# Kernel optimization log

Hardware: AMD Instinct MI355X
Metric: run time of the kernel (lower is better)

The kernel has to match this reference:

```python
import jax, jax.numpy as jnp
import numpy as np

B, S, E, H, F = 4, 1024, 1024, 16, 4096
D = E // H
DEPTH = 3
EPS_LN = 1e-5
EPS_ENT = 1e-6


def setup_inputs() -> dict:
    key = jax.random.key(0)
    ks = jax.random.split(key, 32)
    def w(k, shp, s=0.02):
        return (jax.random.normal(k, shp) * s).astype(jnp.float32)
    z = lambda *shp: jnp.zeros(shp, jnp.float32)
    inp = {
        'x': jax.random.normal(ks[0], (B, S, E), jnp.float32),
        # self-referential attention
        'sr_w': w(ks[1], (E, E)), 'sr_b': z(E),
        'q_w': w(ks[2], (E, E)), 'q_b': z(E),
        'k_w': w(ks[3], (E, E)), 'k_b': z(E),
        'v_w': w(ks[4], (E, E)), 'v_b': z(E),
        'o_w': w(ks[5], (E, E)), 'o_b': z(E),
        'ref_gate': jnp.float32(0.5),
        # quantum-classical interface
        'c_w': w(ks[6], (E, E)), 'c_b': z(E),
        'qp_w': w(ks[7], (E, E)), 'qp_b': z(E),
        'ig_w': w(ks[8], (2 * E, E)), 'ig_b': z(E),
        'temperature': jnp.float32(1.0),
        # entropy regulator
        'kp_w': w(ks[9], (E, E)), 'kp_b': z(E),
        'ee_w': w(ks[10], (E, 1)), 'ee_b': z(1),
        'eta': jnp.float32(0.1),
        # ffn
        'f1_w': w(ks[11], (E, F)), 'f1_b': z(F),
        'f2_w': w(ks[12], (F, E)), 'f2_b': z(E),
        # layernorms
        'ln1_g': jnp.ones(E, jnp.float32), 'ln1_b': z(E),
        'ln2_g': jnp.ones(E, jnp.float32), 'ln2_b': z(E),
        'ln3_g': jnp.ones(E, jnp.float32), 'ln3_b': z(E),
        # observer
        'obs_w': w(ks[13], (E, E)), 'obs_b': z(E),
        'obs_gate': jnp.float32(0.2),
    }
    return inp


def _lin(x, W, b):
    return x @ W + b


def _ln(x, g, b):
    m = jnp.mean(x, -1, keepdims=True)
    v = jnp.var(x, -1, keepdims=True)
    return (x - m) * jax.lax.rsqrt(v + EPS_LN) * g + b


def _layer(x, p):
    ks = jax.lax.stop_gradient(x)  # knowledge_state = x.detach()
    scale = 1.0 / (D ** 0.5)
    for _ in range(DEPTH):  # fixed small recursion depth
        # --- self-referential attention on norm1(x) ---
        xn = _ln(x, p['ln1_g'], p['ln1_b'])
        xr = xn + p['ref_gate'] * _lin(xn, p['sr_w'], p['sr_b'])
        b, s, _ = xn.shape
        q = _lin(xr, p['q_w'], p['q_b']).reshape(b, s, H, D)
        k = _lin(xr, p['k_w'], p['k_b']).reshape(b, s, H, D)
        v = _lin(xn, p['v_w'], p['v_b']).reshape(b, s, H, D)
        scores = jnp.einsum('bqhd,bkhd->bhqk', q, k) * scale  # [B,H,S,S]
        aw = jax.nn.softmax(scores, axis=-1)
        ao = jnp.einsum('bhqk,bkhd->bqhd', aw, v).reshape(b, s, E)
        quantum = _lin(ao, p['o_w'], p['o_b'])
        # --- FFN on norm2(x) (dropout = identity, eval mode) ---
        xn2 = _ln(x, p['ln2_g'], p['ln2_b'])
        h = jax.nn.gelu(_lin(xn2, p['f1_w'], p['f1_b']), approximate=False)
        classical = _lin(h, p['f2_w'], p['f2_b'])
        # --- quantum-classical interface ---
        c_proj = _lin(classical, p['c_w'], p['c_b'])
        q_proj = _lin(quantum, p['qp_w'], p['qp_b'])
        gate = jax.nn.sigmoid(_lin(jnp.concatenate([c_proj, q_proj], -1), p['ig_w'], p['ig_b']))
        sim = jnp.einsum('bqe,bke->bqk', c_proj, q_proj) / (E ** 0.5)  # [B,S,S]
        attw = jax.nn.softmax(sim / p['temperature'], axis=-1)
        transfer = jnp.einsum('bqk,bke->bqe', attw, quantum)
        iface = classical + gate * transfer
        # --- entropy regulator ---
        logp = jax.nn.log_softmax(iface, axis=-1)
        entropy = -jnp.sum(jnp.exp(logp) * logp, -1, keepdims=True)
        neg_entropy = _lin(ks, p['kp_w'], p['kp_b'])
        bal = jax.nn.sigmoid(_lin(iface, p['ee_w'], p['ee_b']))
        regulated = iface + p['eta'] * bal * (neg_entropy / (entropy + EPS_ENT))
        # --- residual + observer feedback + knowledge update ---
        x = x + regulated
        x = x + p['obs_gate'] * _lin(x, p['obs_w'], p['obs_b'])
        ks = ks + 0.1 * (x - ks)
    x = _ln(x, p['ln3_g'], p['ln3_b'])
    return x, ks


def reference(x, sr_w, sr_b, q_w, q_b, k_w, k_b, v_w, v_b, o_w, o_b, ref_gate,
              c_w, c_b, qp_w, qp_b, ig_w, ig_b, temperature,
              kp_w, kp_b, ee_w, ee_b, eta,
              f1_w, f1_b, f2_w, f2_b,
              ln1_g, ln1_b, ln2_g, ln2_b, ln3_g, ln3_b,
              obs_w, obs_b, obs_gate):
    p = dict(sr_w=sr_w, sr_b=sr_b, q_w=q_w, q_b=q_b, k_w=k_w, k_b=k_b,
             v_w=v_w, v_b=v_b, o_w=o_w, o_b=o_b, ref_gate=ref_gate,
             c_w=c_w, c_b=c_b, qp_w=qp_w, qp_b=qp_b, ig_w=ig_w, ig_b=ig_b,
             temperature=temperature, kp_w=kp_w, kp_b=kp_b, ee_w=ee_w, ee_b=ee_b,
             eta=eta, f1_w=f1_w, f1_b=f1_b, f2_w=f2_w, f2_b=f2_b,
             ln1_g=ln1_g, ln1_b=ln1_b, ln2_g=ln2_g, ln2_b=ln2_b,
             ln3_g=ln3_g, ln3_b=ln3_b, obs_w=obs_w, obs_b=obs_b, obs_gate=obs_gate)
    return _layer(x, p)
```

## Files before the change

### kernel.cpp

```cpp
#include <hip/hip_runtime.h>
#include <hip/hip_bf16.h>
#include <cmath>


typedef unsigned short u16;
typedef short v8s __attribute__((ext_vector_type(8)));
typedef float v4f __attribute__((ext_vector_type(4)));
typedef unsigned short u16x4 __attribute__((ext_vector_type(4)));
typedef unsigned int u32x4 __attribute__((ext_vector_type(4)));

#define DEV __device__ __forceinline__

DEV float b2f(u16 u) { return __uint_as_float(((unsigned int)u) << 16); }
DEV u16 f2b(float f) {
    unsigned int x = __float_as_uint(f);
    return (u16)((x + 0x7fffu + ((x >> 16) & 1u)) >> 16);
}
DEV bool badf(float f) { return ((__float_as_uint(f) >> 23) & 0xFF) == 0xFF; }

DEV void async16(const void* g, void* l) {
    __builtin_amdgcn_global_load_lds((const __attribute__((address_space(1))) void*)g,
                                     (__attribute__((address_space(3))) void*)l, 16, 0, 0);
}

struct InArr { const void* p[37]; int n[37]; };
struct BJobs { int si[20]; int off[20]; int n[20]; };
struct GJ2 { const u16* jA; const u16* jB; const u16* jbias; u16* jout; };

#define CLS_CAP 16384

__global__ void reset_k(int* diag, int* cnt) {
    if (threadIdx.x == 0) *diag = 0x7FFFFFFF;
    if (threadIdx.x < 80) cnt[threadIdx.x] = 0;
}

__global__ void classify_k(InArr A, int* cnt) {
    int i = blockIdx.y;
    int n = A.n[i];
    if (n <= 1) return;
    long pairs = (long)n >> 1;
    int wild = 0, pz = 0;
    if (pairs > (long)(2 * CLS_CAP)) {
        const unsigned int* q32 = (const unsigned int*)A.p[i];
        long p0 = ((long)blockIdx.x * (pairs >> 3)) & ~3L;
        long tbase = p0 + (long)threadIdx.x * 8;
#pragma unroll
        for (int c = 0; c < 2; c++) {
            u32x4 v = *(const u32x4*)(q32 + tbase + c * 4);
#pragma unroll
            for (int j = 0; j < 4; j++) {
                unsigned int p = v[j];
                u16 w0 = (u16)(p & 0xFFFFu), w1 = (u16)(p >> 16);
                wild += ((w0 & 0x7FFF) >= 0x5000) + ((w1 & 0x7FFF) >= 0x5000);
                pz += (w0 == 0 && w1 >= 0x3000 && w1 <= 0x4100) ? 1 : 0;
            }
        }
    } else {
        const u16* q = (const u16*)A.p[i];
        long stride = (long)gridDim.x * blockDim.x;
        for (long j = (long)blockIdx.x * blockDim.x + threadIdx.x; j < pairs; j += stride) {
            u16 w0 = q[2 * j], w1 = q[2 * j + 1];
            wild += ((w0 & 0x7FFF) >= 0x5000) + ((w1 & 0x7FFF) >= 0x5000);
            pz += (w0 == 0 && w1 >= 0x3000 && w1 <= 0x4100) ? 1 : 0;
        }
    }
#pragma unroll
    for (int off = 1; off < 64; off <<= 1) {
        wild += __shfl_xor(wild, off);
        pz += __shfl_xor(pz, off);
    }
    if ((threadIdx.x & 63) == 0) {
        atomicAdd(&cnt[2 * i], wild);
        atomicAdd(&cnt[2 * i + 1], pz);
    }
}

__global__ void finalize_k(InArr A, const int* cnt, int* flags) {
    int i = threadIdx.x;
    if (i < 37) {
        int n = A.n[i];
        int f = 0;
        if (n > 1) {
            long pairs = (long)n >> 1;
            long wthr, pthr;
            if (pairs > (long)(2 * CLS_CAP)) { wthr = (2L * CLS_CAP) >> 6; pthr = (long)CLS_CAP >> 2; }
            else { wthr = (long)n >> 6; pthr = (long)n >> 3; }
            f = (cnt[2 * i] > wthr) || (cnt[2 * i + 1] > pthr);
        }
        flags[i] = f;
    }
}

DEV float dec_scalar(const u16* p) {
    float bf = b2f(p[0]);
    if (bf > 0.0009765625f && bf < 8.0f) return bf;
    unsigned int w = (((unsigned int)p[1]) << 16) | (unsigned int)p[0];
    return __uint_as_float(w);
}

__global__ void decode_scalars_k(const u16* rg, const u16* tp, const u16* et,
                                 const u16* og, float* out)
{
    if (threadIdx.x == 0 && blockIdx.x == 0) {
        out[0] = dec_scalar(rg);
        out[1] = dec_scalar(tp);
        out[2] = dec_scalar(et);
        out[3] = dec_scalar(og);
    }
}

__global__ void cvt1d_k(InArr A, BJobs J, const int* flags, u16* BIA) {
    int j = blockIdx.y;
    int n = J.n[j];
    int si = J.si[j];
    const void* src = A.p[si];
    u16* dst = BIA + (long)J.off[j] * 1024;
    int f = flags[si];
    int stride = gridDim.x * blockDim.x;
    for (int i = blockIdx.x * blockDim.x + threadIdx.x; i < n; i += stride) {
        dst[i] = f ? f2b(((const float*)src)[i]) : ((const u16*)src)[i];
    }
}

__global__ void chk_scal_k(const float* scal, int* diag) {
    if (threadIdx.x == 0) {
        for (int i = 0; i < 4; i++) {
            float v = scal[i];
            if (!(v > 0.f && v < 8.f)) atomicMin(diag, 3);
        }
    }
}

__global__ void fin32_k(float* out, long n4, const int* diag) {
    long stride = (long)gridDim.x * blockDim.x;
    long i0 = (long)blockIdx.x * blockDim.x + threadIdx.x;
    v4f* o4 = (v4f*)out;
    for (long i = i0; i < n4; i += stride) {
        v4f v = o4[i];
        bool b = false;
#pragma unroll
        for (int j = 0; j < 4; j++) b |= badf(v[j]);
        if (b) {
#pragma unroll
            for (int j = 0; j < 4; j++) if (badf(v[j])) v[j] = 0.f;
            o4[i] = v;
        }
    }
    if (i0 == 0) {
        int d = *diag;
        if (d != 0x7FFFFFFF) out[0] = 200.f + 4.f * (float)(d < 70 ? d : 70);
    }
}

__global__ void small_k(float* out, int code) {
    if (threadIdx.x == 0 && blockIdx.x == 0) out[0] = 900.f + 4.f * code;
}

__global__ __launch_bounds__(256) void f2c_k(const float* __restrict__ a, const float* __restrict__ b,
                                             const u16* __restrict__ bias, u16* __restrict__ out,
                                             int stage, int* __restrict__ diag)
{
    long i0 = ((long)blockIdx.x * 256 + threadIdx.x) * 4;
    v4f va = *(const v4f*)(a + i0);
    v4f vb = *(const v4f*)(b + i0);
    int colb = (int)(i0 & 1023);
    bool bad = false;
    u16x4 o;
#pragma unroll
    for (int j = 0; j < 4; j++) {
        float r = va[j] + vb[j] + b2f(bias[colb + j]);
        bad |= badf(r);
        o[j] = f2b(r);
    }
    *(u16x4*)(out + i0) = o;
    if (__ballot(bad) && (threadIdx.x & 63) == 0) atomicMin(diag, stage);
}

__global__ __launch_bounds__(256) void igc_k(const float* __restrict__ a, const float* __restrict__ b,
                                             const u16* __restrict__ bias, u16* __restrict__ out,
                                             int stage, int* __restrict__ diag)
{
    long i0 = ((long)blockIdx.x * 256 + threadIdx.x) * 4;
    v4f va = *(const v4f*)(a + i0);
    v4f vb = *(const v4f*)(b + i0);
    int colb = (int)(i0 & 1023);
    bool bad = false;
    u16x4 o;
#pragma unroll
    for (int j = 0; j < 4; j++) {
        float r = 1.f / (1.f + expf(-(va[j] + vb[j] + b2f(bias[colb + j]))));
        bad |= badf(r);
        o[j] = f2b(r);
    }
    *(u16x4*)(out + i0) = o;
    if (__ballot(bad) && (threadIdx.x & 63) == 0) atomicMin(diag, stage);
}

__global__ __launch_bounds__(256) void flashc_k(
    const float* __restrict__ Of, const float* __restrict__ Mf, const float* __restrict__ Lf,
    u16* __restrict__ ao, int stage, int* __restrict__ diag)
{
    long i0 = ((long)blockIdx.x * 256 + threadIdx.x) * 4;
    int row4 = (int)(i0 >> 10);
    int col = (int)(i0 & 1023);
    int b = row4 >> 10, srow = row4 & 1023, h = col >> 6;
    int mli = (((b << 4) + h) << 10) + srow;
    float m0 = Mf[mli], m1 = Mf[65536 + mli];
    float l0 = Lf[mli], l1 = Lf[65536 + mli];
    float m = fmaxf(m0, m1);
    float e0 = __expf(m0 - m), e1 = __expf(m1 - m);
    float inv = 1.f / (l0 * e0 + l1 * e1);
    v4f a = *(const v4f*)(Of + i0);
    v4f bb = *(const v4f*)(Of + 4194304 + i0);
    bool bad = false;
    u16x4 o;
#pragma unroll
    for (int j = 0; j < 4; j++) {
        float val = (a[j] * e0 + bb[j] * e1) * inv;
        bad |= badf(val);
        o[j] = f2b(val);
    }
    *(u16x4*)(ao + i0) = o;
    if (__ballot(bad) && (threadIdx.x & 63) == 0) atomicMin(diag, stage);
}

template <int EPI>
__global__ __launch_bounds__(512) void gemm_bt(
    const u16* __restrict__ A, int lda, long sA,
    const u16* __restrict__ A2, int ksplit,
    const u16* __restrict__ Bt, int ldb, long sB,
    const u16* __restrict__ bias,
    u16* __restrict__ obf, float* __restrict__ of32, int ldc, long sC,
    int K,
    const float* __restrict__ scp,
    const u16* __restrict__ aux,
    float* __restrict__ xaux, float* __restrict__ ksf, u16* __restrict__ ksb,
    float* __restrict__ kso,
    GJ2 J2,
    int stage, int* __restrict__ diag)
{
    __shared__ __align__(16) u16 As[128 * 64];
    __shared__ __align__(16) u16 Bs[128 * 64];
    const int tid = threadIdx.x;
    const int w = tid >> 6, l = tid & 63;
    const int lr = l & 15, lq = l >> 4;

    const int gx = gridDim.x, gy = gridDim.y;
    const int nwg = gx * gy * (int)gridDim.z;
    int flat = blockIdx.x + gx * (blockIdx.y + gy * blockIdx.z);
    int qq = nwg >> 3, rr = nwg & 7;
    int xcd = flat & 7, loc = flat >> 3;
    int nf = (xcd < rr ? xcd * (qq + 1) : rr * (qq + 1) + (xcd - rr) * qq) + loc;
    const int bx = nf % gx;
    int tmp = nf / gx;
    const int by = tmp % gy;
    int z = tmp / gy;

    const u16* Aj = A; const u16* Bj = Bt; const u16* biasj = bias; u16* obfj = obf;
    float* of32j = of32;
    if (J2.jA) {
        int jzs = (int)gridDim.z >> 1;
        if (z >= jzs) {
            Aj = J2.jA; Bj = J2.jB; biasj = J2.jbias;
            if (EPI == 8) of32j = (float*)J2.jout; else obfj = J2.jout;
            z -= jzs;
        }
    }

    const int m0 = by * 128, n0 = bx * 128;
    const u16* Az = Aj + (long)z * sA;
    const u16* Bz = Bj + (long)z * sB;
    const int wm = (w >> 2) * 64, wn = (w & 3) * 32;

    v4f zero4 = {0.f, 0.f, 0.f, 0.f};
    v4f acc[4][2];
#pragma unroll
    for (int i = 0; i < 4; i++)
#pragma unroll
        for (int j = 0; j < 2; j++) acc[i][j] = zero4;

    const int swz = lr & 7;
    const int c0s = (lq ^ swz) << 3;
    const int c1s = ((lq + 4) ^ swz) << 3;
    for (int k0 = 0; k0 < K; k0 += 64) {
        __syncthreads();
        const u16* Ab = (k0 < ksplit) ? (Az + k0) : (A2 + (k0 - ksplit));
#pragma unroll
        for (int p = 0; p < 2; p++) {
            int c = p * 512 + tid;
            int row = c >> 3;
            int sc = ((c & 7) ^ (row & 7)) * 8;
            async16(Ab + (long)(m0 + row) * lda + sc, (char*)As + p * 8192 + w * 1024);
            async16(Bz + (long)(n0 + row) * ldb + k0 + sc, (char*)Bs + p * 8192 + w * 1024);
        }
        __syncthreads();
        v8s av0[4], av1[4], bv0[2], bv1[2];
#pragma unroll
        for (int mi = 0; mi < 4; mi++) {
            const u16* Ar = As + ((wm + mi * 16 + lr) << 6);
            av0[mi] = *(const v8s*)(Ar + c0s);
            av1[mi] = *(const v8s*)(Ar + c1s);
        }
#pragma unroll
        for (int ni = 0; ni < 2; ni++) {
            const u16* Br = Bs + ((wn + ni * 16 + lr) << 6);
            bv0[ni] = *(const v8s*)(Br + c0s);
            bv1[ni] = *(const v8s*)(Br + c1s);
        }
#pragma unroll
        for (int mi = 0; mi < 4; mi++)
#pragma unroll
            for (int ni = 0; ni < 2; ni++)
                acc[mi][ni] = __builtin_amdgcn_mfma_f32_16x16x32_bf16(av0[mi], bv0[ni], acc[mi][ni], 0, 0, 0);
#pragma unroll
        for (int mi = 0; mi < 4; mi++)
#pragma unroll
            for (int ni = 0; ni < 2; ni++)
                acc[mi][ni] = __builtin_amdgcn_mfma_f32_16x16x32_bf16(av1[mi], bv1[ni], acc[mi][ni], 0, 0, 0);
    }

    float gsv = 0.f;
    if (EPI == 5 || EPI == 6) gsv = scp[0];
    bool bad = false;
#pragma unroll
    for (int mi = 0; mi < 4; mi++) {
        int row = m0 + wm + mi * 16 + lq * 4;
#pragma unroll
        for (int ni = 0; ni < 2; ni++) {
            int col = n0 + wn + ni * 16 + lr;
            float bb = biasj ? b2f(biasj[col]) : 0.f;
#pragma unroll
            for (int r = 0; r < 4; r++) {
                float v = acc[mi][ni][r] + bb;
                if (EPI == 6 || EPI == 7) {
                    long rbase = (long)(row + r) * 1024;
                    float res;
                    if (col < 1024) {
                        if (EPI == 6) res = b2f(aux[rbase + col]) + gsv * v;
                        else res = v * 0.125f;
                        bad |= badf(res);
                        obfj[rbase + col] = f2b(res);
                    } else {
                        res = v;
                        bad |= badf(res);
                        J2.jout[rbase + col - 1024] = f2b(res);
                    }
                } else {
                    long idx = (long)z * sC + (long)(row + r) * ldc + col;
                    float res = v;
                    if (EPI == 2) res = 0.5f * v * (1.f + erff(v * 0.70710678118654752f));
                    else if (EPI == 5) {
                        float xv = xaux[idx];
                        float nx = xv + gsv * v;
                        xaux[idx] = nx;
                        float kv = ksf[idx];
                        float kn = kv + 0.1f * (nx - kv);
                        ksf[idx] = kn;
                        ksb[idx] = f2b(kn);
                        if (kso) kso[idx] = kn;
                        bad |= badf(kn);
                        res = nx;
                    }
                    bad |= badf(res);
                    if (obfj) obfj[idx] = f2b(res);
                    if (of32j) of32j[idx] = res;
                }
            }
        }
    }
    if (__ballot(bad) && l == 0) atomicMin(diag, stage);
}

__global__ __launch_bounds__(256) void flash_k(
    const u16* __restrict__ q, const u16* __restrict__ k, const u16* __restrict__ v,
    float* __restrict__ Of, float* __restrict__ Mf, float* __restrict__ Lf)
{
    __shared__ __align__(16) u16 Ks[2 * 64 * 64];
    __shared__ __align__(16) u16 Vt[64 * 64];
    __shared__ __align__(16) u16 Pw[4 * 16 * 64];
    const int tid = threadIdx.x, w = tid >> 6, l = tid & 63;
    const int lr = l & 15, lq = l >> 4;
    const int flat = blockIdx.x + (blockIdx.y << 4) + (blockIdx.z << 10);
    const int xcd = flat & 7, loc = flat >> 3;
    const int bh = xcd * 8 + (loc >> 5);
    const int rest = loc & 31;
    const int zk = rest >> 4;
    const int q0 = (rest & 15) * 64;
    const int b = bh >> 4, h = bh & 15;
    const long rowbase = (long)b * 1024;
    const int h64 = h * 64;
    const long zoff = (long)zk << 19;

    const u16* Qp = q + (rowbase + q0 + w * 16 + lr) * 1024 + h64;
    v8s aq0 = *(const v8s*)(Qp + lq * 8);
    v8s aq1 = *(const v8s*)(Qp + 32 + lq * 8);

    v4f zero4 = {0.f, 0.f, 0.f, 0.f};
    v4f oacc[4];
    float m_r[4], l_r[4];
#pragma unroll
    for (int i = 0; i < 4; i++) { oacc[i] = zero4; m_r[i] = -INFINITY; l_r[i] = 0.f; }

    const int ss = lr & 7;
    const int colk = (lq ^ ss) << 3;
    u16* Pp = Pw + w * (16 * 64);

    const int c0 = tid, c1 = 256 + tid;
    const int row0 = c0 >> 3, cc0 = (c0 & 7) * 8;
    const int row1 = c1 >> 3, cc1 = (c1 & 7) * 8;
    const int sl0 = ((c0 & 7) ^ (row0 & 7)) * 8;
    const int sl1 = ((c1 & 7) ^ (row1 & 7)) * 8;
    int vt0[8], vt1[8];
#pragma unroll
    for (int j = 0; j < 8; j++) {
        int d0 = cc0 + j, g0 = (d0 & 7) ^ ((d0 >> 3) & 7);
        vt0[j] = ((d0 << 6) + row0) ^ (g0 << 3);
        int d1 = cc1 + j, g1 = (d1 & 7) ^ ((d1 >> 3) & 7);
        vt1[j] = ((d1 << 6) + row1) ^ (g1 << 3);
    }
    const u16* kc0 = k + (rowbase + row0) * 1024 + h64 + sl0 + zoff;
    const u16* kc1 = k + (rowbase + row1) * 1024 + h64 + sl1 + zoff;
    const u16* vc0 = v + (rowbase + row0) * 1024 + h64 + cc0 + zoff;
    const u16* vc1 = v + (rowbase + row1) * 1024 + h64 + cc1 + zoff;

    async16(kc0, (char*)Ks + w * 1024);
    async16(kc1, (char*)Ks + 4096 + w * 1024);
    v8s vv0 = *(const v8s*)vc0;
    v8s vv1 = *(const v8s*)vc1;
    v8s vvn0 = vv0, vvn1 = vv1;
    int cur = 0;

    for (int kt = 0; kt < 8; kt++) {
        __syncthreads();
        const long koff = (long)(kt + 1) << 16;
        if (kt < 7) {
            int nb = (cur ^ 1) * 8192;
            async16(kc0 + koff, (char*)Ks + nb + w * 1024);
            async16(kc1 + koff, (char*)Ks + nb + 4096 + w * 1024);
            vvn0 = *(const v8s*)(vc0 + koff);
            vvn1 = *(const v8s*)(vc1 + koff);
        }
        const u16* Kb = Ks + cur * 4096;

        v4f s[4];
#pragma unroll
        for (int nt = 0; nt < 4; nt++) {
            const u16* Kr = Kb + ((nt * 16 + lr) << 6);
            v8s b0 = *(const v8s*)(Kr + colk);
            v8s b1 = *(const v8s*)(Kr + (colk ^ 32));
            v4f t = zero4;
            t = __builtin_amdgcn_mfma_f32_16x16x32_bf16(aq0, b0, t, 0, 0, 0);
            t = __builtin_amdgcn_mfma_f32_16x16x32_bf16(aq1, b1, t, 0, 0, 0);
            s[nt] = t;
        }
#pragma unroll
        for (int r = 0; r < 4; r++) {
            float mx = fmaxf(fmaxf(s[0][r], s[1][r]), fmaxf(s[2][r], s[3][r]));
#pragma unroll
            for (int off = 1; off < 16; off <<= 1) mx = fmaxf(mx, __shfl_xor(mx, off));
            float mn = fmaxf(m_r[r], mx);
            float al = __expf(m_r[r] - mn);
            float rs = 0.f;
            int qrow = lq * 4 + r;
            int pbase = qrow << 6;
            int pswz = (qrow & 7) << 3;
#pragma unroll
            for (int nt = 0; nt < 4; nt++) {
                float pv = __expf(s[nt][r] - mn);
                rs += pv;
                Pp[pbase + ((nt * 16 + lr) ^ pswz)] = f2b(pv);
            }
#pragma unroll
            for (int off = 1; off < 16; off <<= 1) rs += __shfl_xor(rs, off);
            l_r[r] = l_r[r] * al + rs;
            m_r[r] = mn;
#pragma unroll
            for (int nt = 0; nt < 4; nt++) oacc[nt][r] *= al;
        }
#pragma unroll
        for (int j = 0; j < 8; j++) {
            Vt[vt0[j]] = (u16)vv0[j];
            Vt[vt1[j]] = (u16)vv1[j];
        }
        __syncthreads();
        const u16* Pr = Pp + (lr << 6);
        v8s pa0 = *(const v8s*)(Pr + colk);
        v8s pa1 = *(const v8s*)(Pr + (colk ^ 32));
#pragma unroll
        for (int nt = 0; nt < 4; nt++) {
            const u16* Vr = Vt + ((nt * 16 + lr) << 6);
            int gv = (ss ^ (2 * nt + (lr >> 3))) << 3;
            int colv = (lq << 3) ^ gv;
            v8s vb0 = *(const v8s*)(Vr + colv);
            v8s vb1 = *(const v8s*)(Vr + (colv ^ 32));
            oacc[nt] = __builtin_amdgcn_mfma_f32_16x16x32_bf16(pa0, vb0, oacc[nt], 0, 0, 0);
            oacc[nt] = __builtin_amdgcn_mfma_f32_16x16x32_bf16(pa1, vb1, oacc[nt], 0, 0, 0);
        }
        vv0 = vvn0; vv1 = vvn1;
        cur ^= 1;
    }
    float* Ofz = Of + (long)zk * 4194304;
#pragma unroll
    for (int r = 0; r < 4; r++) {
        int srow = q0 + w * 16 + lq * 4 + r;
#pragma unroll
        for (int nt = 0; nt < 4; nt++) {
            Ofz[(rowbase + srow) * 1024 + h64 + nt * 16 + lr] = oacc[nt][r];
        }
        if (lr == 0) {
            int mli = zk * 65536 + (bh << 10) + srow;
            Mf[mli] = m_r[r];
            Lf[mli] = l_r[r];
        }
    }
}

template <int F32OUT>
__global__ __launch_bounds__(256) void ln_k(const float* __restrict__ x,
                                            const u16* __restrict__ g, const u16* __restrict__ bt,
                                            u16* __restrict__ outb, float* __restrict__ outf,
                                            int stage, int* __restrict__ diag)
{
    __shared__ float red[8];
    int row = blockIdx.x, t = threadIdx.x, w = t >> 6;
    const float* xr = x + (long)row * 1024;
    float v[4], s = 0.f, sq = 0.f;
#pragma unroll
    for (int i = 0; i < 4; i++) { v[i] = xr[i * 256 + t]; s += v[i]; sq += v[i] * v[i]; }
#pragma unroll
    for (int off = 1; off < 64; off <<= 1) { s += __shfl_xor(s, off); sq += __shfl_xor(sq, off); }
    if ((t & 63) == 0) { red[w] = s; red[4 + w] = sq; }
    __syncthreads();
    float S = red[0] + red[1] + red[2] + red[3];
    float SQ = red[4] + red[5] + red[6] + red[7];
    float mean = S * (1.f / 1024.f);
    float var = fmaxf(SQ * (1.f / 1024.f) - mean * mean, 0.f);
    float rs = rsqrtf(var + 1e-5f);
    bool bad = false;
#pragma unroll
    for (int i = 0; i < 4; i++) {
        int e = i * 256 + t;
        float r = (v[i] - mean) * rs * b2f(g[e]) + b2f(bt[e]);
        bad |= badf(r);
        if (F32OUT) outf[(long)row * 1024 + e] = r;
        else outb[(long)row * 1024 + e] = f2b(r);
    }
    if (__ballot(bad) && (t & 63) == 0) atomicMin(diag, stage);
}

__global__ __launch_bounds__(256) void ln12_k(const float* __restrict__ x,
                                              const u16* __restrict__ g1, const u16* __restrict__ b1,
                                              const u16* __restrict__ g2, const u16* __restrict__ b2,
                                              u16* __restrict__ out1, u16* __restrict__ out2,
                                              int stage, int* __restrict__ diag)
{
    __shared__ float red[8];
    int row = blockIdx.x, t = threadIdx.x, w = t >> 6;
    const float* xr = x + (long)row * 1024;
    float v[4], s = 0.f, sq = 0.f;
#pragma unroll
    for (int i = 0; i < 4; i++) { v[i] = xr[i * 256 + t]; s += v[i]; sq += v[i] * v[i]; }
#pragma unroll
    for (int off = 1; off < 64; off <<= 1) { s += __shfl_xor(s, off); sq += __shfl_xor(sq, off); }
    if ((t & 63) == 0) { red[w] = s; red[4 + w] = sq; }
    __syncthreads();
    float S = red[0] + red[1] + red[2] + red[3];
    float SQ = red[4] + red[5] + red[6] + red[7];
    float mean = S * (1.f / 1024.f);
    float var = fmaxf(SQ * (1.f / 1024.f) - mean * mean, 0.f);
    float rs = rsqrtf(var + 1e-5f);
    bool bad = false;
#pragma unroll
    for (int i = 0; i < 4; i++) {
        int e = i * 256 + t;
        float nv = (v[i] - mean) * rs;
        float r1 = nv * b2f(g1[e]) + b2f(b1[e]);
        float r2 = nv * b2f(g2[e]) + b2f(b2[e]);
        bad |= badf(r1) | badf(r2);
        out1[(long)row * 1024 + e] = f2b(r1);
        out2[(long)row * 1024 + e] = f2b(r2);
    }
    if (__ballot(bad) && (t & 63) == 0) atomicMin(diag, stage);
}

__global__ __launch_bounds__(256) void rowfuse_k(
    const u16* __restrict__ cls, const u16* __restrict__ gate,
    const float* __restrict__ tra, const float* __restrict__ trb,
    const u16* __restrict__ ne, const u16* __restrict__ eew, const u16* __restrict__ eeb,
    const float* __restrict__ eta_p, float* __restrict__ xbuf, u16* __restrict__ x1b,
    int stage, int* __restrict__ diag)
{
    __shared__ float red[16];
    int row = blockIdx.x, t = threadIdx.x, w = t >> 6;
    long base = (long)row * 1024;
    float ifc[4];
#pragma unroll
    for (int i = 0; i < 4; i++) {
        int e = i * 256 + t;
        ifc[i] = b2f(cls[base + e]) + b2f(gate[base + e]) * (tra[base + e] + trb[base + e]);
    }
    float mx = fmaxf(fmaxf(ifc[0], ifc[1]), fmaxf(ifc[2], ifc[3]));
#pragma unroll
    for (int off = 1; off < 64; off <<= 1) mx = fmaxf(mx, __shfl_xor(mx, off));
    if ((t & 63) == 0) red[w] = mx;
    __syncthreads();
    float MX = fmaxf(fmaxf(red[0], red[1]), fmaxf(red[2], red[3]));
    float s1 = 0.f, s2 = 0.f, dot = 0.f;
#pragma unroll
    for (int i = 0; i < 4; i++) {
        int e = i * 256 + t;
        float ex = expf(ifc[i] - MX);
        s1 += ex; s2 += ex * ifc[i]; dot += ifc[i] * b2f(eew[e]);
    }
#pragma unroll
    for (int off = 1; off < 64; off <<= 1) {
        s1 += __shfl_xor(s1, off); s2 += __shfl_xor(s2, off); dot += __shfl_xor(dot, off);
    }
    if ((t & 63) == 0) { red[4 + w] = s1; red[8 + w] = s2; red[12 + w] = dot; }
    __syncthreads();
    float S1 = red[4] + red[5] + red[6] + red[7];
    float S2 = red[8] + red[9] + red[10] + red[11];
    float DT = red[12] + red[13] + red[14] + red[15];
    float logZ = MX + logf(S1);
    float ent = logZ - S2 / S1;
    float bal = 1.f / (1.f + expf(-(DT + b2f(eeb[0]))));
    float fac = eta_p[0] * bal / (ent + 1e-6f);
    bool bad = false;
#pragma unroll
    for (int i = 0; i < 4; i++) {
        int e = i * 256 + t;
        float rg = ifc[i] + fac * b2f(ne[base + e]);
        float x1 = xbuf[base + e] + rg;
        bad |= badf(x1);
        xbuf[base + e] = x1;
        x1b[base + e] = f2b(x1);
    }
    if (__ballot(bad) && (t & 63) == 0) atomicMin(diag, stage);
}

__global__ __launch_bounds__(256) void softmax_k(const float* __restrict__ pa, const float* __restrict__ pb,
                                                 const float* __restrict__ tp, u16* __restrict__ out,
                                                 int stage, int* __restrict__ diag)
{
    __shared__ float red[8];
    int row = blockIdx.x, t = threadIdx.x, w = t >> 6;
    long base = (long)row * 1024;
    float sc = 0.03125f / fmaxf(tp[0], 1e-8f);
    float v[4];
#pragma unroll
    for (int i = 0; i < 4; i++) v[i] = (pa[base + i * 256 + t] + pb[base + i * 256 + t]) * sc;
    float mx = fmaxf(fmaxf(v[0], v[1]), fmaxf(v[2], v[3]));
#pragma unroll
    for (int off = 1; off < 64; off <<= 1) mx = fmaxf(mx, __shfl_xor(mx, off));
    if ((t & 63) == 0) red[w] = mx;
    __syncthreads();
    float MX = fmaxf(fmaxf(red[0], red[1]), fmaxf(red[2], red[3]));
    float s = 0.f;
#pragma unroll
    for (int i = 0; i < 4; i++) { v[i] = expf(v[i] - MX); s += v[i]; }
#pragma unroll
    for (int off = 1; off < 64; off <<= 1) s += __shfl_xor(s, off);
    if ((t & 63) == 0) red[4 + w] = s;
    __syncthreads();
    float inv = 1.f / (red[4] + red[5] + red[6] + red[7]);
    bool bad = false;
#pragma unroll
    for (int i = 0; i < 4; i++) {
        float o = v[i] * inv;
        bad |= badf(o);
        out[base + i * 256 + t] = f2b(o);
    }
    if (__ballot(bad) && (t & 63) == 0) atomicMin(diag, stage);
}

__global__ void transpose_ft_k(const void* __restrict__ in, u16* __restrict__ out,
                               int R, int C, const int* __restrict__ flags, int idx,
                               int* __restrict__ diag)
{
    __shared__ u16 tile[32][33];
    int f = flags[idx];
    int x = blockIdx.x * 32 + threadIdx.x;
    int y0 = blockIdx.y * 32;
#pragma unroll
    for (int j = 0; j < 4; j++) {
        long src = (long)(y0 + threadIdx.y + j * 8) * C + x;
        tile[threadIdx.y + j * 8][threadIdx.x] =
            f ? f2b(((const float*)in)[src]) : ((const u16*)in)[src];
    }
    __syncthreads();
    int ox = y0 + threadIdx.x;
    int oy0 = blockIdx.x * 32;
    bool bad = false;
#pragma unroll
    for (int j = 0; j < 4; j++) {
        u16 u = tile[threadIdx.x][threadIdx.y + j * 8];
        bad |= ((u & 0x7FFF) >= 0x7F80);
        out[(long)(oy0 + threadIdx.y + j * 8) * R + ox] = u;
    }
    if (__ballot(bad) && ((threadIdx.y * 32 + threadIdx.x) & 63) == 0) atomicMin(diag, 2);
}

__global__ void transpose_k(const u16* __restrict__ in, u16* __restrict__ out,
                            int R, int C, long sIn, long sOut)
{
    __shared__ u16 tile[32][33];
    int z = blockIdx.z;
    in += (long)z * sIn; out += (long)z * sOut;
    int x = blockIdx.x * 32 + threadIdx.x;
    int y0 = blockIdx.y * 32;
#pragma unroll
    for (int j = 0; j < 4; j++)
        tile[threadIdx.y + j * 8][threadIdx.x] = in[(long)(y0 + threadIdx.y + j * 8) * C + x];
    __syncthreads();
    int ox = y0 + threadIdx.x;
    int oy0 = blockIdx.x * 32;
#pragma unroll
    for (int j = 0; j < 4; j++)
        out[(long)(oy0 + threadIdx.y + j * 8) * R + ox] = tile[threadIdx.x][threadIdx.y + j * 8];
}

__global__ __launch_bounds__(256) void init_k(const void* __restrict__ xin, const int* __restrict__ flags,
                                              float* __restrict__ xbuf,
                                              float* __restrict__ ksf, u16* __restrict__ ksb,
                                              int* __restrict__ diag)
{
    int t = threadIdx.x;
    int f = flags[0];
    long base = (long)blockIdx.x * 1024;
    bool bad = false;
#pragma unroll
    for (int i = 0; i < 4; i++) {
        long idx = base + i * 256 + t;
        float xv = f ? ((const float*)xin)[idx] : b2f(((const u16*)xin)[idx]);
        bad |= badf(xv);
        xbuf[idx] = xv; ksf[idx] = xv; ksb[idx] = f2b(xv);
    }
    if (__ballot(bad) && (t & 63) == 0) atomicMin(diag, 1);
}

extern "C" void kernel_launch(void* const* d_in, const int* in_sizes, int n_in,
                              void* d_out, int out_size, void* d_ws, size_t ws_size,
                              hipStream_t stream)
{
    const size_t MB = 1u << 20;
    float* outf = (float*)d_out;
    if (ws_size < 192 * MB) {
        int code = (int)(ws_size >> 25); if (code > 9) code = 9;
        small_k<<<1, 64, 0, stream>>>(outf, code);
        return;
    }
    const u16* s_refg = (const u16*)d_in[11];
    const u16* s_temp = (const u16*)d_in[18];
    const u16* s_eta  = (const u16*)d_in[23];
    const u16* s_obsg = (const u16*)d_in[36];

    InArr IA;
    for (int i = 0; i < 37; i++) { IA.p[i] = d_in[i]; IA.n[i] = (i < n_in) ? in_sizes[i] : 0; }

    char* ws = (char*)d_ws;
    u16* srT  = (u16*)(ws + 0 * MB);
    u16* vT   = (u16*)(ws + 2 * MB);
    u16* qT   = (u16*)(ws + 4 * MB);
    u16* kT   = (u16*)(ws + 6 * MB);
    u16* oT   = (u16*)(ws + 8 * MB);
    u16* cT   = (u16*)(ws + 10 * MB);
    u16* qpT  = (u16*)(ws + 12 * MB);
    u16* kpT  = (u16*)(ws + 14 * MB);
    u16* obsT = (u16*)(ws + 16 * MB);
    u16* igT  = (u16*)(ws + 18 * MB);
    u16* f1T  = (u16*)(ws + 22 * MB);
    u16* f2T  = (u16*)(ws + 30 * MB);
    float* scal = (float*)(ws + 38 * MB);
    int* diag  = (int*)(ws + 38 * MB + 64);
    int* flags = (int*)(ws + 38 * MB + 128);
    int* cnt   = (int*)(ws + 38 * MB + 512);
    u16* BIA   = (u16*)(ws + 38 * MB + 8192);
    u16* c_bsr = BIA + 0*1024,  *c_bv = BIA + 1*1024;
    u16* c_bq  = BIA + 2*1024,  *c_bk = BIA + 3*1024;
    u16* c_bo  = BIA + 4*1024,  *c_bc = BIA + 5*1024;
    u16* c_bqp = BIA + 6*1024,  *c_big = BIA + 7*1024, *c_bkp = BIA + 8*1024;
    u16* c_bobs= BIA + 9*1024,  *c_bf2 = BIA + 10*1024;
    u16* c_g1  = BIA + 11*1024, *c_be1 = BIA + 12*1024;
    u16* c_g2  = BIA + 13*1024, *c_be2 = BIA + 14*1024;
    u16* c_g3  = BIA + 15*1024, *c_be3 = BIA + 16*1024;
    u16* c_eew = BIA + 17*1024, *c_eeb = BIA + 18*1024;
    u16* c_bf1 = BIA + 19*1024;
    float* Mf = (float*)(ws + 39 * MB);
    float* Lf = (float*)(ws + 39 * MB + 524288);
    float* xbuf = (float*)(ws + 40 * MB);
    float* ksf  = (float*)(ws + 56 * MB);
    u16* ksb    = (u16*)(ws + 72 * MB);
    u16* xn     = (u16*)(ws + 80 * MB);
    u16* xn2    = (u16*)(ws + 88 * MB);
    u16* xr     = (u16*)(ws + 96 * MB);
    u16* qb     = (u16*)(ws + 104 * MB);
    u16* kb     = (u16*)(ws + 112 * MB);
    u16* vb     = (u16*)(ws + 120 * MB);
    u16* aob    = (u16*)(ws + 128 * MB);
    u16* quant  = (u16*)(ws + 136 * MB);
    u16* hb     = (u16*)(ws + 144 * MB);
    u16* clsb   = (u16*)(ws + 176 * MB);
    u16* neb    = (u16*)(ws + 184 * MB);
    float* f2pa = (float*)(ws + 104 * MB);
    float* f2pb = (float*)(ws + 120 * MB);
    float* ppa  = (float*)(ws + 144 * MB);
    float* ppb  = (float*)(ws + 160 * MB);
    u16* quantT = xn;
    u16* cpb = qb;  u16* qpb = kb;  u16* gateb = vb;  u16* attw = aob;  u16* x1b = xr;

    const long BS1 = 1024L * 1024L;
    const int KBIG = 1 << 30;
    dim3 tb(32, 8), blk(256), gblk(512);
    GJ2 J0 = {nullptr, nullptr, nullptr, nullptr};

    auto G = [&](int epi, int gx, int gy, int gz,
                 const u16* A, int lda, long sA, const u16* A2, int ksp,
                 const u16* Bt, int ldb, long sB, const u16* bias,
                 u16* obf, float* of32, int ldc, long sC, int K,
                 const float* scp, const u16* aux, float* xa, float* kf, u16* kb2, float* kso,
                 GJ2 J2, int stg) {
        dim3 grid(gx, gy, gz);
        switch (epi) {
            case 0: gemm_bt<0><<<grid, gblk, 0, stream>>>(A, lda, sA, A2, ksp, Bt, ldb, sB, bias, obf, of32, ldc, sC, K, scp, aux, xa, kf, kb2, kso, J2, stg, diag); break;
            case 2: gemm_bt<2><<<grid, gblk, 0, stream>>>(A, lda, sA, A2, ksp, Bt, ldb, sB, bias, obf, of32, ldc, sC, K, scp, aux, xa, kf, kb2, kso, J2, stg, diag); break;
            case 5: gemm_bt<5><<<grid, gblk, 0, stream>>>(A, lda, sA, A2, ksp, Bt, ldb, sB, bias, obf, of32, ldc, sC, K, scp, aux, xa, kf, kb2, kso, J2, stg, diag); break;
            case 6: gemm_bt<6><<<grid, gblk, 0, stream>>>(A, lda, sA, A2, ksp, Bt, ldb, sB, bias, obf, of32, ldc, sC, K, scp, aux, xa, kf, kb2, kso, J2, stg, diag); break;
            case 7: gemm_bt<7><<<grid, gblk, 0, stream>>>(A, lda, sA, A2, ksp, Bt, ldb, sB, bias, obf, of32, ldc, sC, K, scp, aux, xa, kf, kb2, kso, J2, stg, diag); break;
            case 8: gemm_bt<8><<<grid, gblk, 0, stream>>>(A, lda, sA, A2, ksp, Bt, ldb, sB, bias, obf, of32, ldc, sC, K, scp, aux, xa, kf, kb2, kso, J2, stg, diag); break;
        }
    };

    reset_k<<<1, 256, 0, stream>>>(diag, cnt);
    classify_k<<<dim3(8, 37), blk, 0, stream>>>(IA, cnt);
    finalize_k<<<1, 64, 0, stream>>>(IA, cnt, flags);
    decode_scalars_k<<<1, 64, 0, stream>>>(s_refg, s_temp, s_eta, s_obsg, scal);
    BJobs BJ = {
        {2, 8, 4, 6, 10, 13, 15, 17, 20, 35, 27, 28, 29, 30, 31, 32, 33, 21, 22, 25},
        {0, 1, 2, 3, 4, 5, 6, 7, 8, 9, 10, 11, 12, 13, 14, 15, 16, 17, 18, 19},
        {1024,1024,1024,1024,1024,1024,1024,1024,1024,1024,1024,1024,1024,1024,1024,1024,1024,1024,1,4096}
    };
    cvt1d_k<<<dim3(4, 20), blk, 0, stream>>>(IA, BJ, flags, BIA);
    struct WT { int idx; u16* dst; long n; int R, C, gx, gy; };
    WT wts[12] = {
        {1, srT, 1048576, 1024, 1024, 32, 32},  {7, vT, 1048576, 1024, 1024, 32, 32},
        {3, qT, 1048576, 1024, 1024, 32, 32},   {5, kT, 1048576, 1024, 1024, 32, 32},
        {9, oT, 1048576, 1024, 1024, 32, 32},   {12, cT, 1048576, 1024, 1024, 32, 32},
        {14, qpT, 1048576, 1024, 1024, 32, 32}, {19, kpT, 1048576, 1024, 1024, 32, 32},
        {34, obsT, 1048576, 1024, 1024, 32, 32},
        {16, igT, 2097152, 2048, 1024, 32, 64},
        {24, f1T, 4194304, 1024, 4096, 128, 32},
        {26, f2T, 4194304, 4096, 1024, 32, 128},
    };
    for (int i = 0; i < 12; i++) {
        transpose_ft_k<<<dim3(wts[i].gx, wts[i].gy, 1), tb, 0, stream>>>(
            d_in[wts[i].idx], wts[i].dst, wts[i].R, wts[i].C, flags, wts[i].idx, diag);
    }
    init_k<<<4096, blk, 0, stream>>>(d_in[0], flags, xbuf, ksf, ksb, diag);
    chk_scal_k<<<1, 64, 0, stream>>>(scal, diag);

    for (int it = 0; it < 3; it++) {
        int sb = 4 + it * 20;
        ln12_k<<<4096, blk, 0, stream>>>(xbuf, c_g1, c_be1, c_g2, c_be2, xn, xn2, sb + 0, diag);
        GJ2 Jsrv = {nullptr, nullptr, nullptr, vb};
        G(6, 16, 32, 1, xn, 1024, 0, nullptr, KBIG, srT, 1024, 0, c_bsr, xr, nullptr, 1024, 0, 1024, scal + 0, xn, nullptr, nullptr, nullptr, nullptr, Jsrv, sb + 1);
        GJ2 Jqk = {nullptr, nullptr, nullptr, kb};
        G(7, 16, 32, 1, xr, 1024, 0, nullptr, KBIG, qT, 1024, 0, c_bq, qb, nullptr, 1024, 0, 1024, nullptr, nullptr, nullptr, nullptr, nullptr, nullptr, Jqk, sb + 2);
        flash_k<<<dim3(16, 64, 2), blk, 0, stream>>>(qb, kb, vb, ppa, Mf, Lf);
        flashc_k<<<4096, blk, 0, stream>>>(ppa, Mf, Lf, aob, sb + 5, diag);
        GJ2 Jokp = {ksb, kpT, c_bkp, neb};
        G(0, 8, 32, 2, aob, 1024, 0, nullptr, KBIG, oT, 1024, 0, c_bo, quant, nullptr, 1024, 0, 1024, nullptr, nullptr, nullptr, nullptr, nullptr, nullptr, Jokp, sb + 6);
        transpose_k<<<dim3(32, 32, 4), tb, 0, stream>>>(quant, quantT, 1024, 1024, BS1, BS1);
        G(2, 32, 32, 1, xn2, 1024, 0, nullptr, KBIG, f1T, 1024, 0, c_bf1, hb, nullptr, 4096, 0, 1024, nullptr, nullptr, nullptr, nullptr, nullptr, nullptr, J0, sb + 8);
        G(8, 8, 32, 2, hb, 4096, 2048, nullptr, KBIG, f2T, 4096, 2048, nullptr, nullptr, f2pa, 1024, 4194304, 2048, nullptr, nullptr, nullptr, nullptr, nullptr, nullptr, J0, sb + 9);
        f2c_k<<<4096, blk, 0, stream>>>(f2pa, f2pb, c_bf2, clsb, sb + 9, diag);
        GJ2 Jcqp = {quant, qpT, c_bqp, qpb};
        G(0, 8, 32, 2, clsb, 1024, 0, nullptr, KBIG, cT, 1024, 0, c_bc, cpb, nullptr, 1024, 0, 1024, nullptr, nullptr, nullptr, nullptr, nullptr, nullptr, Jcqp, sb + 10);
        GJ2 Jig = {qpb, igT + 1024, nullptr, (u16*)ppb};
        G(8, 8, 32, 2, cpb, 1024, 0, nullptr, KBIG, igT, 2048, 0, nullptr, nullptr, ppa, 1024, 0, 1024, nullptr, nullptr, nullptr, nullptr, nullptr, nullptr, Jig, sb + 12);
        igc_k<<<4096, blk, 0, stream>>>(ppa, ppb, c_big, gateb, sb + 12, diag);
        GJ2 Jsim = {cpb + 512, qpb + 512, nullptr, (u16*)ppb};
        G(8, 8, 8, 8, cpb, 1024, BS1, nullptr, KBIG, qpb, 1024, BS1, nullptr, nullptr, ppa, 1024, BS1, 512, nullptr, nullptr, nullptr, nullptr, nullptr, nullptr, Jsim, sb + 14);
        softmax_k<<<4096, blk, 0, stream>>>(ppa, ppb, scal + 1, attw, sb + 15, diag);
        GJ2 Jtrf = {attw + 512, quantT + 512, nullptr, (u16*)ppb};
        G(8, 8, 8, 8, attw, 1024, BS1, nullptr, KBIG, quantT, 1024, BS1, nullptr, nullptr, ppa, 1024, BS1, 512, nullptr, nullptr, nullptr, nullptr, nullptr, nullptr, Jtrf, sb + 16);
        rowfuse_k<<<4096, blk, 0, stream>>>(clsb, gateb, ppa, ppb, neb, c_eew, c_eeb, scal + 2, xbuf, x1b, sb + 17, diag);
        float* kso = (it == 2) ? (outf + 4194304) : nullptr;
        G(5, 8, 32, 1, x1b, 1024, 0, nullptr, KBIG, obsT, 1024, 0, c_bobs, nullptr, nullptr, 1024, 0, 1024, scal + 3, nullptr, xbuf, ksf, ksb, kso, J0, sb + 18);
    }
    ln_k<1><<<4096, blk, 0, stream>>>(xbuf, c_g3, c_be3, nullptr, outf, 70, diag);
    fin32_k<<<1024, blk, 0, stream>>>(outf, 2097152, diag);
}
```

Baseline: 1.588 ms.

## Double-buffer LDS tiles in gemm_bt to overlap global loads with MFMA

Doubles the shared-memory A/B tiles and prefetches the next K-slice with async global-to-LDS loads while the current slice is consumed by MFMAs. Each iteration now has one barrier instead of two. The intent is to hide global load latency behind compute. In exchange LDS use doubles to 64KB per block, which may cut occupancy. A single barrier per iteration also relies on the async loads having completed by the time of that barrier.

```diff
diff --git a/kernel.cpp b/kernel.cpp
--- a/kernel.cpp
+++ b/kernel.cpp
@@ -239,8 +239,8 @@
     GJ2 J2,
     int stage, int* __restrict__ diag)
 {
-    __shared__ __align__(16) u16 As[128 * 64];
-    __shared__ __align__(16) u16 Bs[128 * 64];
+    __shared__ __align__(16) u16 As[2 * 128 * 64];
+    __shared__ __align__(16) u16 Bs[2 * 128 * 64];
     const int tid = threadIdx.x;
     const int w = tid >> 6, l = tid & 63;
     const int lr = l & 15, lq = l >> 4;
@@ -282,28 +282,45 @@
     const int swz = lr & 7;
     const int c0s = (lq ^ swz) << 3;
     const int c1s = ((lq + 4) ^ swz) << 3;
+    const int srow = tid >> 3;
+    const int ssc = (((tid & 7) ^ (srow & 7)) * 8);
+    const int sdst = w * 1024 + (l & 63) * 0;
+
+    {
+        const u16* Ab = (0 < ksplit) ? Az : A2;
+#pragma unroll
+        for (int p = 0; p < 2; p++) {
+            int row = p * 64 + srow;
+            async16(Ab + (long)(m0 + row) * lda + ssc, (char*)As + p * 8192 + w * 1024);
+            async16(Bz + (long)(n0 + row) * ldb + ssc, (char*)Bs + p * 8192 + w * 1024);
+        }
+    }
+    __syncthreads();
+    int cur = 0;
     for (int k0 = 0; k0 < K; k0 += 64) {
-        __syncthreads();
-        const u16* Ab = (k0 < ksplit) ? (Az + k0) : (A2 + (k0 - ksplit));
-#pragma unroll
-        for (int p = 0; p < 2; p++) {
-            int c = p * 512 + tid;
-            int row = c >> 3;
-            int sc = ((c & 7) ^ (row & 7)) * 8;
-            async16(Ab + (long)(m0 + row) * lda + sc, (char*)As + p * 8192 + w * 1024);
-            async16(Bz + (long)(n0 + row) * ldb + k0 + sc, (char*)Bs + p * 8192 + w * 1024);
-        }
-        __syncthreads();
+        int kn = k0 + 64;
+        if (kn < K) {
+            const u16* Ab = (kn < ksplit) ? (Az + kn) : (A2 + (kn - ksplit));
+            int nb = (cur ^ 1) * 16384;
+#pragma unroll
+            for (int p = 0; p < 2; p++) {
+                int row = p * 64 + srow;
+                async16(Ab + (long)(m0 + row) * lda + ssc, (char*)As + nb + p * 8192 + w * 1024);
+                async16(Bz + (long)(n0 + row) * ldb + kn + ssc, (char*)Bs + nb + p * 8192 + w * 1024);
+            }
+        }
+        const u16* Asc = As + cur * 8192;
+        const u16* Bsc = Bs + cur * 8192;
         v8s av0[4], av1[4], bv0[2], bv1[2];
 #pragma unroll
         for (int mi = 0; mi < 4; mi++) {
-            const u16* Ar = As + ((wm + mi * 16 + lr) << 6);
+            const u16* Ar = Asc + ((wm + mi * 16 + lr) << 6);
             av0[mi] = *(const v8s*)(Ar + c0s);
             av1[mi] = *(const v8s*)(Ar + c1s);
         }
 #pragma unroll
         for (int ni = 0; ni < 2; ni++) {
-            const u16* Br = Bs + ((wn + ni * 16 + lr) << 6);
+            const u16* Br = Bsc + ((wn + ni * 16 + lr) << 6);
             bv0[ni] = *(const v8s*)(Br + c0s);
             bv1[ni] = *(const v8s*)(Br + c1s);
         }
@@ -317,6 +334,8 @@
 #pragma unroll
             for (int ni = 0; ni < 2; ni++)
                 acc[mi][ni] = __builtin_amdgcn_mfma_f32_16x16x32_bf16(av1[mi], bv1[ni], acc[mi][ni], 0, 0, 0);
+        __syncthreads();
+        cur ^= 1;
     }
 
     float gsv = 0.f;
```

After: 1.520 ms. 1.04x faster.
